# Kernel tuning notes

Hardware: AMD Instinct MI355X
Metric: run time of the kernel (lower is better)

The kernel has to match this reference:

```python
import jax, jax.numpy as jnp
import numpy as np

NUM_HEADS = 12
HEAD_DIM = 64
LOGIT_SCALE_MAX = 4.605170185988092  # log(1/0.01), open_clip default
EPS = 1e-12  # F.normalize eps


def setup_inputs() -> dict:
    key = jax.random.key(0)
    ks = jax.random.split(key, 8)
    N, L, C = 2, 2048, 768
    return {
        "x": jax.random.normal(ks[0], (N, L, C), dtype=jnp.float32),
        "in_proj_w": jax.random.normal(ks[1], (3 * C, C), dtype=jnp.float32) * 0.02,
        "in_proj_b": jax.random.normal(ks[2], (3 * C,), dtype=jnp.float32) * 0.02,
        "logit_scale": jax.random.normal(ks[3], (NUM_HEADS, 1, 1), dtype=jnp.float32),
        "learned_scale": jnp.ones((NUM_HEADS,), dtype=jnp.float32),
        "out_proj_w": jax.random.normal(ks[4], (C, C), dtype=jnp.float32) * 0.02,
        "out_proj_b": jax.random.normal(ks[5], (C,), dtype=jnp.float32) * 0.02,
        "attn_mask": jnp.zeros((L, L), dtype=jnp.float32),
    }


def _l2norm(t):
    # F.normalize(dim=-1): x / max(||x||, eps)
    n = jnp.linalg.norm(t, axis=-1, keepdims=True)
    return t / jnp.maximum(n, EPS)


def reference(x, in_proj_w, in_proj_b, logit_scale, learned_scale,
              out_proj_w, out_proj_b, attn_mask):
    N, L, C = x.shape
    H, D = NUM_HEADS, HEAD_DIM
    # packed QKV projection: [N, L, 3C]
    qkv = jnp.einsum("nlc,fc->nlf", x, in_proj_w) + in_proj_b
    q, k, v = jnp.split(qkv, 3, axis=-1)
    # [N, L, C] -> [N, H, L, D]
    to_heads = lambda t: t.reshape(N, L, H, D).transpose(0, 2, 1, 3)
    q, k, v = to_heads(q), to_heads(k), to_heads(v)
    # cosine attention with clamped exp logit scale per head
    attn = jnp.einsum("nhld,nhmd->nhlm", _l2norm(q), _l2norm(k))
    ls = jnp.exp(jnp.minimum(logit_scale, LOGIT_SCALE_MAX))  # [H,1,1]
    attn = attn * ls[None]  # broadcast over [N,H,L,L]
    attn = attn + attn_mask  # additive mask [L,L]
    attn = jax.nn.softmax(attn, axis=-1)
    out = jnp.einsum("nhlm,nhmd->nhld", attn, v)
    # learned per-head output scale
    out = out * learned_scale[None, :, None, None]
    # [N,H,L,D] -> [N,L,C]
    out = out.transpose(0, 2, 1, 3).reshape(N, L, C)
    out = jnp.einsum("nlc,fc->nlf", out, out_proj_w) + out_proj_b
    return out
```

## Files before the change

kernel.cpp:

```cpp
#include <hip/hip_runtime.h>
#include <math.h>

#define NB   2
#define SEQ  2048
#define CH   768
#define NH   12
#define HD   64
#define F3   2304
#define LSMAX 4.605170185988092f
#define LOG2E 1.4426950408889634f

typedef _Float16 f16;
typedef __attribute__((ext_vector_type(8))) _Float16 f16x8;
typedef __attribute__((ext_vector_type(4))) _Float16 f16x4;
typedef __attribute__((ext_vector_type(2))) _Float16 f16x2;
typedef __attribute__((ext_vector_type(4))) float f32x4;

#define QSZ   3145728
#define OATT  (3 * QSZ)
#define XHOFF 12582912
#define W1OFF 15728640
#define W2OFF 17498112
#define FLAGO 18087936

#define KP   72
#define VP   136
#define PPIT 76
#define GP   40
#define GP2  72

__global__ __launch_bounds__(256) void cvt_f16(const float* __restrict__ X,
                                               const float* __restrict__ W1,
                                               const float* __restrict__ W2,
                                               const float* __restrict__ M,
                                               f16* __restrict__ Xh,
                                               f16* __restrict__ W1h,
                                               f16* __restrict__ W2h,
                                               int* __restrict__ flag)
{
    int tid = blockIdx.x * 256 + threadIdx.x;
    if (blockIdx.y == 3) {
        if (tid < 1048576) {
            float4 v = ((const float4*)M)[tid];
            bool nz = (v.x != 0.f) || (v.y != 0.f) || (v.z != 0.f) || (v.w != 0.f);
            if (__any(nz) && (threadIdx.x & 63) == 0) atomicOr(flag, 1);
        }
        return;
    }
    const float* src; f16* dst; int n4;
    switch (blockIdx.y) {
        case 0:  src = X;  dst = Xh;  n4 = 786432;  break;
        case 1:  src = W1; dst = W1h; n4 = 442368;  break;
        default: src = W2; dst = W2h; n4 = 147456;  break;
    }
    if (tid < n4) {
        float4 v = ((const float4*)src)[tid];
        f16x4 o = {(f16)v.x, (f16)v.y, (f16)v.z, (f16)v.w};
        ((f16x4*)dst)[tid] = o;
    }
}

__global__ __launch_bounds__(256, 4) void qkv_gemm(const f16* __restrict__ Xh,
                                                   const f16* __restrict__ Wh,
                                                   const float* __restrict__ bias,
                                                   const float* __restrict__ logit_scale,
                                                   f16* __restrict__ qkv16)
{
    __shared__ f16 As[128 * GP];
    __shared__ f16 Bs[128 * GP];
    const int t    = threadIdx.x;
    const int w    = t >> 6;
    const int lane = t & 63;
    const int quad = lane >> 4;
    const int sub  = lane & 15;
    const int wm   = w & 1, wn = w >> 1;
    const int f0   = blockIdx.x * 128;
    const int m0   = blockIdx.y * 128;
    const int srow = t >> 1;
    const int sk   = (t & 1) * 16;

    const f16* ag = Xh + (size_t)(m0 + srow) * CH + sk;
    const f16* bg = Wh + (size_t)(f0 + srow) * CH + sk;
    f16x8 a0 = *(const f16x8*)(ag);
    f16x8 a1 = *(const f16x8*)(ag + 8);
    f16x8 b0 = *(const f16x8*)(bg);
    f16x8 b1 = *(const f16x8*)(bg + 8);

    f32x4 acc[4][4];
#pragma unroll
    for (int i = 0; i < 4; ++i)
#pragma unroll
        for (int j = 0; j < 4; ++j) acc[i][j] = (f32x4){0.f, 0.f, 0.f, 0.f};

    for (int k0 = 0; k0 < CH; k0 += 32) {
        __syncthreads();
        *(f16x8*)&As[srow * GP + sk + 0] = a0;
        *(f16x8*)&As[srow * GP + sk + 8] = a1;
        *(f16x8*)&Bs[srow * GP + sk + 0] = b0;
        *(f16x8*)&Bs[srow * GP + sk + 8] = b1;
        __syncthreads();
        if (k0 + 32 < CH) {
            a0 = *(const f16x8*)(ag + k0 + 32);
            a1 = *(const f16x8*)(ag + k0 + 40);
            b0 = *(const f16x8*)(bg + k0 + 32);
            b1 = *(const f16x8*)(bg + k0 + 40);
        }
        f16x8 af[4], bf[4];
#pragma unroll
        for (int i = 0; i < 4; ++i) {
            af[i] = *(const f16x8*)&As[(wm * 64 + i * 16 + sub) * GP + quad * 8];
            bf[i] = *(const f16x8*)&Bs[(wn * 64 + i * 16 + sub) * GP + quad * 8];
        }
#pragma unroll
        for (int i = 0; i < 4; ++i)
#pragma unroll
            for (int j = 0; j < 4; ++j)
                acc[i][j] = __builtin_amdgcn_mfma_f32_16x16x32_f16(af[i], bf[j], acc[i][j], 0, 0, 0);
    }

    const int t3 = f0 / CH;
    const int h  = ((f0 + wn * 64) % CH) >> 6;
    f16* dst = qkv16 + (size_t)t3 * QSZ;
    float lsv = (t3 == 0) ? __expf(fminf(logit_scale[h], LSMAX)) * LOG2E : 1.0f;
    float bb[4];
#pragma unroll
    for (int j = 0; j < 4; ++j) bb[j] = bias[f0 + wn * 64 + j * 16 + sub];
#pragma unroll
    for (int i = 0; i < 4; ++i) {
#pragma unroll
        for (int r = 0; r < 4; ++r) {
            int m = m0 + wm * 64 + i * 16 + quad * 4 + r;
            int n = m >> 11, l = m & 2047;
            float v[4];
#pragma unroll
            for (int j = 0; j < 4; ++j) v[j] = acc[i][j][r] + bb[j];
            float scale = 1.0f;
            if (t3 < 2) {
                float ss = v[0] * v[0] + v[1] * v[1] + v[2] * v[2] + v[3] * v[3];
#pragma unroll
                for (int mk = 1; mk < 16; mk <<= 1) ss += __shfl_xor(ss, mk, 64);
                scale = 1.0f / fmaxf(sqrtf(ss), 1e-12f);
                if (t3 == 0) scale *= lsv;
            }
            f16* drow = dst + (((size_t)n * NH + h) * SEQ + l) * HD;
#pragma unroll
            for (int j = 0; j < 4; ++j)
                drow[j * 16 + sub] = (f16)(v[j] * scale);
        }
    }
}

__global__ __launch_bounds__(256, 3) void attn(const f16* __restrict__ Qh,
                                               const f16* __restrict__ Kh,
                                               const f16* __restrict__ Vh,
                                               const float* __restrict__ M32,
                                               const float* __restrict__ lscale,
                                               const int* __restrict__ flag,
                                               f16* __restrict__ Og)
{
    __shared__ f16 Ks[128 * KP];
    __shared__ f16 Vt[64 * VP];
    __shared__ f16 QP[64 * PPIT];

    const int t    = threadIdx.x;
    const int w    = t >> 6;
    const int lane = t & 63;
    const int quad = lane >> 4;
    const int sub  = lane & 15;
    const int qb   = blockIdx.x * 64;
    const int h    = blockIdx.y, n = blockIdx.z;
    const bool has_mask = (*flag) != 0;

    const f16* Qg = Qh + ((size_t)(n * NH + h) * SEQ + qb) * HD;
    const f16* Kg = Kh + (size_t)(n * NH + h) * SEQ * HD;
    const f16* Vg = Vh + (size_t)(n * NH + h) * SEQ * HD;
    const float* Mg = M32 + (size_t)(qb + w * 16 + quad * 4) * SEQ;

#pragma unroll
    for (int rep = 0; rep < 2; ++rep) {
        int id = rep * 256 + t;
        int row = id >> 3, c8 = id & 7;
        f16x8 v = *(const f16x8*)&Qg[row * 64 + c8 * 8];
        *(f16x4*)&QP[row * PPIT + c8 * 8 + 0] = (f16x4){v[0], v[1], v[2], v[3]};
        *(f16x4*)&QP[row * PPIT + c8 * 8 + 4] = (f16x4){v[4], v[5], v[6], v[7]};
    }

    const int krow = t >> 1;
    const int kcb  = (t & 1) * 32;
    f16x8 kr0, kr1, kr2, kr3, vr0, vr1, vr2, vr3;
    {
        const f16* kp = Kg + krow * 64 + kcb;
        kr0 = *(const f16x8*)(kp + 0);
        kr1 = *(const f16x8*)(kp + 8);
        kr2 = *(const f16x8*)(kp + 16);
        kr3 = *(const f16x8*)(kp + 24);
        const f16* vp = Vg + (2 * lane) * 64 + w * 16;
        vr0 = *(const f16x8*)(vp + 0);
        vr1 = *(const f16x8*)(vp + 8);
        vr2 = *(const f16x8*)(vp + 64);
        vr3 = *(const f16x8*)(vp + 72);
    }

    __syncthreads();
    f16x8 qf0, qf1;
    {
        f16x4 l0 = *(const f16x4*)&QP[(w * 16 + sub) * PPIT + quad * 8];
        f16x4 l1 = *(const f16x4*)&QP[(w * 16 + sub) * PPIT + quad * 8 + 4];
        f16x4 l2 = *(const f16x4*)&QP[(w * 16 + sub) * PPIT + 32 + quad * 8];
        f16x4 l3 = *(const f16x4*)&QP[(w * 16 + sub) * PPIT + 32 + quad * 8 + 4];
        qf0 = (f16x8){l0[0], l0[1], l0[2], l0[3], l1[0], l1[1], l1[2], l1[3]};
        qf1 = (f16x8){l2[0], l2[1], l2[2], l2[3], l3[0], l3[1], l3[2], l3[3]};
    }

    {
        f16* kd = &Ks[krow * KP + kcb];
        *(f16x8*)(kd + 0)  = kr0;
        *(f16x8*)(kd + 8)  = kr1;
        *(f16x8*)(kd + 16) = kr2;
        *(f16x8*)(kd + 24) = kr3;
#pragma unroll
        for (int j = 0; j < 8; ++j) {
            *(f16x2*)&Vt[(w * 16 + j) * VP + 2 * lane]     = (f16x2){vr0[j], vr2[j]};
            *(f16x2*)&Vt[(w * 16 + 8 + j) * VP + 2 * lane] = (f16x2){vr1[j], vr3[j]};
        }
    }
    __syncthreads();

    const f16x8 ones = {(f16)1.f, (f16)1.f, (f16)1.f, (f16)1.f,
                        (f16)1.f, (f16)1.f, (f16)1.f, (f16)1.f};
    f32x4 o[4];
    f32x4 l_acc = (f32x4){0.f, 0.f, 0.f, 0.f};
    float m_run[4];
#pragma unroll
    for (int dt = 0; dt < 4; ++dt) o[dt] = (f32x4){0.f, 0.f, 0.f, 0.f};
#pragma unroll
    for (int r = 0; r < 4; ++r) m_run[r] = -1e30f;

    const int NITER = SEQ / 128;
    for (int c = 0; c < NITER; ++c) {
        const int c0 = c * 128;
        if (c + 1 < NITER) {
            const f16* kp = Kg + (c0 + 128 + krow) * 64 + kcb;
            kr0 = *(const f16x8*)(kp + 0);
            kr1 = *(const f16x8*)(kp + 8);
            kr2 = *(const f16x8*)(kp + 16);
            kr3 = *(const f16x8*)(kp + 24);
            const f16* vp = Vg + (c0 + 128 + 2 * lane) * 64 + w * 16;
            vr0 = *(const f16x8*)(vp + 0);
            vr1 = *(const f16x8*)(vp + 8);
            vr2 = *(const f16x8*)(vp + 64);
            vr3 = *(const f16x8*)(vp + 72);
        }

        f32x4 s[8];
#pragma unroll
        for (int ct = 0; ct < 8; ++ct) {
            f16x8 kf0 = *(const f16x8*)&Ks[(ct * 16 + sub) * KP + quad * 8];
            f16x8 kf1 = *(const f16x8*)&Ks[(ct * 16 + sub) * KP + 32 + quad * 8];
            f32x4 a = (f32x4){0.f, 0.f, 0.f, 0.f};
            a = __builtin_amdgcn_mfma_f32_16x16x32_f16(qf0, kf0, a, 0, 0, 0);
            a = __builtin_amdgcn_mfma_f32_16x16x32_f16(qf1, kf1, a, 0, 0, 0);
            s[ct] = a;
        }
        if (has_mask) {
#pragma unroll
            for (int ct = 0; ct < 8; ++ct)
#pragma unroll
                for (int r = 0; r < 4; ++r)
                    s[ct][r] += LOG2E * Mg[(size_t)r * SEQ + c0 + ct * 16 + sub];
        }
        float mnew[4];
#pragma unroll
        for (int r = 0; r < 4; ++r) {
            float a01 = fmaxf(s[0][r], s[1][r]), a23 = fmaxf(s[2][r], s[3][r]);
            float a45 = fmaxf(s[4][r], s[5][r]), a67 = fmaxf(s[6][r], s[7][r]);
            mnew[r] = fmaxf(fmaxf(fmaxf(a01, a23), fmaxf(a45, a67)), m_run[r]);
        }
        {
            union { f16x2 h; int i; } p0, p1, v0, v1;
            p0.h = (f16x2){(f16)mnew[0], (f16)mnew[1]};
            p1.h = (f16x2){(f16)mnew[2], (f16)mnew[3]};
#pragma unroll
            for (int mk = 1; mk < 16; mk <<= 1) {
                v0.i = __shfl_xor(p0.i, mk, 64);
                v1.i = __shfl_xor(p1.i, mk, 64);
                p0.h = __builtin_elementwise_max(p0.h, v0.h);
                p1.h = __builtin_elementwise_max(p1.h, v1.h);
            }
            mnew[0] = (float)p0.h[0]; mnew[1] = (float)p0.h[1];
            mnew[2] = (float)p1.h[0]; mnew[3] = (float)p1.h[1];
        }
        float alpha[4];
#pragma unroll
        for (int r = 0; r < 4; ++r) {
            alpha[r] = exp2f(m_run[r] - mnew[r]);
            m_run[r] = mnew[r];
        }
#pragma unroll
        for (int dt = 0; dt < 4; ++dt)
#pragma unroll
            for (int r = 0; r < 4; ++r) o[dt][r] *= alpha[r];
#pragma unroll
        for (int r = 0; r < 4; ++r) l_acc[r] *= alpha[r];

#pragma unroll
        for (int hf = 0; hf < 2; ++hf) {
#pragma unroll
            for (int ct = 0; ct < 4; ++ct)
#pragma unroll
                for (int r = 0; r < 4; ++r) {
                    float p = exp2f(s[hf * 4 + ct][r] - mnew[r]);
                    QP[(w * 16 + quad * 4 + r) * PPIT + ct * 16 + sub] = (f16)p;
                }
            f16x4 p00 = *(const f16x4*)&QP[(w * 16 + sub) * PPIT + quad * 8];
            f16x4 p01 = *(const f16x4*)&QP[(w * 16 + sub) * PPIT + quad * 8 + 4];
            f16x4 p10 = *(const f16x4*)&QP[(w * 16 + sub) * PPIT + 32 + quad * 8];
            f16x4 p11 = *(const f16x4*)&QP[(w * 16 + sub) * PPIT + 32 + quad * 8 + 4];
            f16x8 pf0 = {p00[0], p00[1], p00[2], p00[3], p01[0], p01[1], p01[2], p01[3]};
            f16x8 pf1 = {p10[0], p10[1], p10[2], p10[3], p11[0], p11[1], p11[2], p11[3]};
            l_acc = __builtin_amdgcn_mfma_f32_16x16x32_f16(pf0, ones, l_acc, 0, 0, 0);
            l_acc = __builtin_amdgcn_mfma_f32_16x16x32_f16(pf1, ones, l_acc, 0, 0, 0);
#pragma unroll
            for (int dt = 0; dt < 4; ++dt) {
                f16x8 vf0 = *(const f16x8*)&Vt[(dt * 16 + sub) * VP + hf * 64 + quad * 8];
                f16x8 vf1 = *(const f16x8*)&Vt[(dt * 16 + sub) * VP + hf * 64 + 32 + quad * 8];
                o[dt] = __builtin_amdgcn_mfma_f32_16x16x32_f16(pf0, vf0, o[dt], 0, 0, 0);
                o[dt] = __builtin_amdgcn_mfma_f32_16x16x32_f16(pf1, vf1, o[dt], 0, 0, 0);
            }
        }

        if (c + 1 < NITER) {
            __syncthreads();
            f16* kd = &Ks[krow * KP + kcb];
            *(f16x8*)(kd + 0)  = kr0;
            *(f16x8*)(kd + 8)  = kr1;
            *(f16x8*)(kd + 16) = kr2;
            *(f16x8*)(kd + 24) = kr3;
#pragma unroll
            for (int j = 0; j < 8; ++j) {
                *(f16x2*)&Vt[(w * 16 + j) * VP + 2 * lane]     = (f16x2){vr0[j], vr2[j]};
                *(f16x2*)&Vt[(w * 16 + 8 + j) * VP + 2 * lane] = (f16x2){vr1[j], vr3[j]};
            }
            __syncthreads();
        }
    }
    float lsc = lscale[h];
#pragma unroll
    for (int r = 0; r < 4; ++r) {
        float inv = lsc / l_acc[r];
        int q = qb + w * 16 + quad * 4 + r;
#pragma unroll
        for (int dt = 0; dt < 4; ++dt)
            Og[((size_t)n * SEQ + q) * CH + h * 64 + dt * 16 + sub] =
                (f16)(o[dt][r] * inv);
    }
}

__global__ __launch_bounds__(256, 4) void out_gemm(const f16* __restrict__ A,
                                                   const f16* __restrict__ Wh,
                                                   const float* __restrict__ bias,
                                                   float* __restrict__ out)
{
    __shared__ f16 As[64 * GP2];
    __shared__ f16 Bs[64 * GP2];
    const int t    = threadIdx.x;
    const int w    = t >> 6;
    const int lane = t & 63;
    const int quad = lane >> 4;
    const int sub  = lane & 15;
    const int f0   = blockIdx.x * 64;
    const int m0   = blockIdx.y * 64;
    const int srow = t >> 2;
    const int sk   = (t & 3) * 16;

    const f16* ag = A + (size_t)(m0 + srow) * CH + sk;
    const f16* bg = Wh + (size_t)(f0 + srow) * CH + sk;
    f16x8 a0 = *(const f16x8*)(ag);
    f16x8 a1 = *(const f16x8*)(ag + 8);
    f16x8 b0 = *(const f16x8*)(bg);
    f16x8 b1 = *(const f16x8*)(bg + 8);

    f32x4 acc[4];
#pragma unroll
    for (int i = 0; i < 4; ++i) acc[i] = (f32x4){0.f, 0.f, 0.f, 0.f};

    for (int k0 = 0; k0 < CH; k0 += 64) {
        __syncthreads();
        *(f16x8*)&As[srow * GP2 + sk + 0] = a0;
        *(f16x8*)&As[srow * GP2 + sk + 8] = a1;
        *(f16x8*)&Bs[srow * GP2 + sk + 0] = b0;
        *(f16x8*)&Bs[srow * GP2 + sk + 8] = b1;
        __syncthreads();
        if (k0 + 64 < CH) {
            a0 = *(const f16x8*)(ag + k0 + 64);
            a1 = *(const f16x8*)(ag + k0 + 72);
            b0 = *(const f16x8*)(bg + k0 + 64);
            b1 = *(const f16x8*)(bg + k0 + 72);
        }
#pragma unroll
        for (int kk = 0; kk < 64; kk += 32) {
            f16x8 bf = *(const f16x8*)&Bs[(w * 16 + sub) * GP2 + kk + quad * 8];
#pragma unroll
            for (int i = 0; i < 4; ++i) {
                f16x8 af = *(const f16x8*)&As[(i * 16 + sub) * GP2 + kk + quad * 8];
                acc[i] = __builtin_amdgcn_mfma_f32_16x16x32_f16(af, bf, acc[i], 0, 0, 0);
            }
        }
    }
    float bb = bias[f0 + w * 16 + sub];
#pragma unroll
    for (int i = 0; i < 4; ++i)
#pragma unroll
        for (int r = 0; r < 4; ++r) {
            int m = m0 + i * 16 + quad * 4 + r;
            out[(size_t)m * CH + f0 + w * 16 + sub] = acc[i][r] + bb;
        }
}

extern "C" void kernel_launch(void* const* d_in, const int* in_sizes, int n_in,
                              void* d_out, int out_size, void* d_ws, size_t ws_size,
                              hipStream_t stream) {
    const float* x    = (const float*)d_in[0];
    const float* w1   = (const float*)d_in[1];
    const float* b1   = (const float*)d_in[2];
    const float* ls   = (const float*)d_in[3];
    const float* lrn  = (const float*)d_in[4];
    const float* w2   = (const float*)d_in[5];
    const float* b2   = (const float*)d_in[6];
    const float* msk  = (const float*)d_in[7];
    f16*   ws16 = (f16*)d_ws;
    int*   flag = (int*)(ws16 + FLAGO);
    float* out  = (float*)d_out;

    (void)hipMemsetAsync(flag, 0, 4, stream);
    hipLaunchKernelGGL(cvt_f16, dim3(4096, 4), dim3(256), 0, stream,
                       x, w1, w2, msk,
                       ws16 + XHOFF, ws16 + W1OFF, ws16 + W2OFF, flag);
    hipLaunchKernelGGL(qkv_gemm, dim3(F3 / 128, (NB * SEQ) / 128), dim3(256), 0, stream,
                       ws16 + XHOFF, ws16 + W1OFF, b1, ls, ws16);
    hipLaunchKernelGGL(attn, dim3(SEQ / 64, NH, NB), dim3(256), 0, stream,
                       ws16, ws16 + QSZ, ws16 + 2 * QSZ, msk, lrn, flag,
                       ws16 + OATT);
    hipLaunchKernelGGL(out_gemm, dim3(CH / 64, (NB * SEQ) / 64), dim3(256), 0, stream,
                       ws16 + OATT, ws16 + W2OFF, b2, out);
}
```

Baseline: 209.6 us.

## Use direct global-to-LDS loads with double buffering and XOR swizzle in QKV GEMM

The QKV projection GEMM now loads its A/B tiles straight from global memory into LDS with global_load_lds, skipping the register staging step. LDS tiles are double-buffered, so the next K-slice loads while MFMAs run on the current one, and each iteration needs one barrier instead of two. Padding is replaced by an XOR swizzle of 8-element chunks, which keeps reads bank-conflict-free with a tighter layout. The risk is correctness if the swizzle or the async-load ordering relative to the barrier is wrong, since there is no explicit vmcnt wait before the syncthreads.

```diff
diff --git a/kernel.cpp b/kernel.cpp
--- a/kernel.cpp
+++ b/kernel.cpp
@@ -16,6 +16,9 @@
 typedef __attribute__((ext_vector_type(2))) _Float16 f16x2;
 typedef __attribute__((ext_vector_type(4))) float f32x4;
 
+typedef __attribute__((address_space(3))) void lds_void;
+typedef __attribute__((address_space(1))) const void gbl_cvoid;
+
 #define QSZ   3145728
 #define OATT  (3 * QSZ)
 #define XHOFF 12582912
@@ -26,7 +29,6 @@
 #define KP   72
 #define VP   136
 #define PPIT 76
-#define GP   40
 #define GP2  72
 
 __global__ __launch_bounds__(256) void cvt_f16(const float* __restrict__ X,
@@ -66,8 +68,8 @@
                                                    const float* __restrict__ logit_scale,
                                                    f16* __restrict__ qkv16)
 {
-    __shared__ f16 As[128 * GP];
-    __shared__ f16 Bs[128 * GP];
+    __shared__ f16 As[2][128 * 32];
+    __shared__ f16 Bs[2][128 * 32];
     const int t    = threadIdx.x;
     const int w    = t >> 6;
     const int lane = t & 63;
@@ -76,15 +78,14 @@
     const int wm   = w & 1, wn = w >> 1;
     const int f0   = blockIdx.x * 128;
     const int m0   = blockIdx.y * 128;
-    const int srow = t >> 1;
-    const int sk   = (t & 1) * 16;
-
-    const f16* ag = Xh + (size_t)(m0 + srow) * CH + sk;
-    const f16* bg = Wh + (size_t)(f0 + srow) * CH + sk;
-    f16x8 a0 = *(const f16x8*)(ag);
-    f16x8 a1 = *(const f16x8*)(ag + 8);
-    f16x8 b0 = *(const f16x8*)(bg);
-    f16x8 b1 = *(const f16x8*)(bg + 8);
+
+    const int s0 = t, s1 = 256 + t;
+    const int r0 = s0 >> 2, cb0 = ((s0 & 3) ^ (r0 & 3)) * 8;
+    const int r1 = s1 >> 2, cb1 = ((s1 & 3) ^ (r1 & 3)) * 8;
+    const f16* ga0 = Xh + (size_t)(m0 + r0) * CH + cb0;
+    const f16* ga1 = Xh + (size_t)(m0 + r1) * CH + cb1;
+    const f16* gb0 = Wh + (size_t)(f0 + r0) * CH + cb0;
+    const f16* gb1 = Wh + (size_t)(f0 + r1) * CH + cb1;
 
     f32x4 acc[4][4];
 #pragma unroll
@@ -92,30 +93,34 @@
 #pragma unroll
         for (int j = 0; j < 4; ++j) acc[i][j] = (f32x4){0.f, 0.f, 0.f, 0.f};
 
+    const int pch = (quad ^ (sub & 3)) * 8;
+
+    __builtin_amdgcn_global_load_lds((gbl_cvoid*)(ga0), (lds_void*)&As[0][s0 * 8], 16, 0, 0);
+    __builtin_amdgcn_global_load_lds((gbl_cvoid*)(ga1), (lds_void*)&As[0][s1 * 8], 16, 0, 0);
+    __builtin_amdgcn_global_load_lds((gbl_cvoid*)(gb0), (lds_void*)&Bs[0][s0 * 8], 16, 0, 0);
+    __builtin_amdgcn_global_load_lds((gbl_cvoid*)(gb1), (lds_void*)&Bs[0][s1 * 8], 16, 0, 0);
+    __syncthreads();
+
     for (int k0 = 0; k0 < CH; k0 += 32) {
-        __syncthreads();
-        *(f16x8*)&As[srow * GP + sk + 0] = a0;
-        *(f16x8*)&As[srow * GP + sk + 8] = a1;
-        *(f16x8*)&Bs[srow * GP + sk + 0] = b0;
-        *(f16x8*)&Bs[srow * GP + sk + 8] = b1;
-        __syncthreads();
+        const int cur = (k0 >> 5) & 1, nxt = cur ^ 1;
         if (k0 + 32 < CH) {
-            a0 = *(const f16x8*)(ag + k0 + 32);
-            a1 = *(const f16x8*)(ag + k0 + 40);
-            b0 = *(const f16x8*)(bg + k0 + 32);
-            b1 = *(const f16x8*)(bg + k0 + 40);
+            __builtin_amdgcn_global_load_lds((gbl_cvoid*)(ga0 + k0 + 32), (lds_void*)&As[nxt][s0 * 8], 16, 0, 0);
+            __builtin_amdgcn_global_load_lds((gbl_cvoid*)(ga1 + k0 + 32), (lds_void*)&As[nxt][s1 * 8], 16, 0, 0);
+            __builtin_amdgcn_global_load_lds((gbl_cvoid*)(gb0 + k0 + 32), (lds_void*)&Bs[nxt][s0 * 8], 16, 0, 0);
+            __builtin_amdgcn_global_load_lds((gbl_cvoid*)(gb1 + k0 + 32), (lds_void*)&Bs[nxt][s1 * 8], 16, 0, 0);
         }
         f16x8 af[4], bf[4];
 #pragma unroll
         for (int i = 0; i < 4; ++i) {
-            af[i] = *(const f16x8*)&As[(wm * 64 + i * 16 + sub) * GP + quad * 8];
-            bf[i] = *(const f16x8*)&Bs[(wn * 64 + i * 16 + sub) * GP + quad * 8];
+            af[i] = *(const f16x8*)&As[cur][(wm * 64 + i * 16 + sub) * 32 + pch];
+            bf[i] = *(const f16x8*)&Bs[cur][(wn * 64 + i * 16 + sub) * 32 + pch];
         }
 #pragma unroll
         for (int i = 0; i < 4; ++i)
 #pragma unroll
             for (int j = 0; j < 4; ++j)
                 acc[i][j] = __builtin_amdgcn_mfma_f32_16x16x32_f16(af[i], bf[j], acc[i][j], 0, 0, 0);
+        __syncthreads();
     }
 
     const int t3 = f0 / CH;
```

Result: no change. 207.7 us (-0.9%).
